# Kernel tuning notes

Measured on AMD Instinct MI355X. Metric: run time of the kernel, lower is better.

## Reference

```python
import jax, jax.numpy as jnp
import numpy as np

N, F_IN, F_OUT = 8192, 256, 128


def setup_inputs() -> dict:
    key = jax.random.key(0)
    k1, k2, k3, k4 = jax.random.split(key, 4)
    h = jax.random.normal(k1, (N, F_IN), dtype=jnp.float32)
    adj = jax.random.randint(k2, (N, N), 0, 2, dtype=jnp.int32)
    # xavier-uniform-like init scales
    w_lim = float(np.sqrt(6.0 / (F_IN + F_OUT)))
    a_lim = float(np.sqrt(6.0 / (2 * F_OUT + 1)))
    W = jax.random.uniform(k3, (F_IN, F_OUT), jnp.float32, -w_lim, w_lim)
    a = jax.random.uniform(k4, (2 * F_OUT, 1), jnp.float32, -a_lim, a_lim)
    return {"h": h, "adj": adj, "W": W, "a": a}


def reference(h, adj, W, a):
    # Wh: [N, F_OUT]
    Wh = h @ W
    # Fused form of the pairwise-concat score: e[i,j] = leakyrelu(Wh_i.a1 + Wh_j.a2)
    a1 = a[:F_OUT]   # [F_OUT, 1]
    a2 = a[F_OUT:]   # [F_OUT, 1]
    s1 = Wh @ a1     # [N, 1]
    s2 = Wh @ a2     # [N, 1]
    e = jax.nn.leaky_relu(s1 + s2.T, negative_slope=0.2)  # [N, N]
    e = jnp.where(adj > 0, e, jnp.float32(-9e15))
    attention = jax.nn.softmax(e, axis=1)
    return attention @ Wh  # [N, F_OUT]
```

## Files before the change

kernel.cpp:

```cpp
#include <hip/hip_runtime.h>

#define N_   8192
#define FIN  256
#define FOUT 128
#define NW   (N_ / 32)

typedef _Float16 f16x8  __attribute__((ext_vector_type(8)));
typedef _Float16 f16x4  __attribute__((ext_vector_type(4)));
typedef float    f32x16 __attribute__((ext_vector_type(16)));
typedef unsigned int uint;

__global__ __launch_bounds__(256) void k_pack(
    const int* __restrict__ adj, uint* __restrict__ bm)
{
    const int wid = (blockIdx.x * 256 + threadIdx.x) >> 6;
    const int l   = threadIdx.x & 63;
    const int4* __restrict__ arow = (const int4*)(adj + (size_t)wid * N_);
    uint* __restrict__ brow = bm + (size_t)wid * NW;

    #pragma unroll 2
    for (int jb = 0; jb < 32; ++jb) {
        int4 av = arow[jb * 64 + l];
        uint nib = (uint)(av.x != 0) | ((uint)(av.y != 0) << 1)
                 | ((uint)(av.z != 0) << 2) | ((uint)(av.w != 0) << 3);
        uint v = nib | (__shfl_xor(nib, 1, 64) << 4);
        v = v | (__shfl_xor(v, 2, 64) << 8);
        v = v | (__shfl_xor(v, 4, 64) << 16);
        if ((l & 7) == 0)
            brow[jb * 8 + (l >> 3)] = v;
    }
}

__global__ __launch_bounds__(256) void k_wh(
    const float* __restrict__ h, const float* __restrict__ W,
    const float* __restrict__ a, float* __restrict__ Wh,
    float* __restrict__ s1, float* __restrict__ s2)
{
    __shared__ float hrow[2][FIN];
    __shared__ float rbuf[2][2][2];
    const int t   = threadIdx.x;
    const int rh  = t >> 7;
    const int c   = t & 127;
    const int row = (blockIdx.x << 1) + rh;

    hrow[rh][c]       = h[(size_t)row * FIN + c];
    hrow[rh][c + 128] = h[(size_t)row * FIN + c + 128];
    __syncthreads();

    float acc = 0.f;
    #pragma unroll 8
    for (int k = 0; k < FIN; ++k)
        acc = fmaf(hrow[rh][k], W[k * FOUT + c], acc);

    Wh[(size_t)row * FOUT + c] = acc;

    float p1 = acc * a[c];
    float p2 = acc * a[FOUT + c];
    #pragma unroll
    for (int off = 32; off; off >>= 1) {
        p1 += __shfl_down(p1, off, 64);
        p2 += __shfl_down(p2, off, 64);
    }
    if ((t & 63) == 0) { rbuf[rh][c >> 6][0] = p1; rbuf[rh][c >> 6][1] = p2; }
    __syncthreads();
    if (c == 0) {
        const float k2 = 1.44269504088896f;
        s1[row] = (rbuf[rh][0][0] + rbuf[rh][1][0]) * k2;
        s2[row] = (rbuf[rh][0][1] + rbuf[rh][1][1]) * k2;
    }
}

__global__ __launch_bounds__(256) void k_tr(
    const float* __restrict__ Wh, _Float16* __restrict__ WhTt)
{
    __shared__ float tile[64][129];
    const int t = threadIdx.x;
    const int rbase = blockIdx.x * 64;

    #pragma unroll
    for (int q = 0; q < 8; ++q) {
        int i4 = q * 256 + t;
        int r  = i4 >> 5;
        int c4 = (i4 & 31) * 4;
        *(float4*)&tile[r][c4] = *(const float4*)&Wh[(size_t)(rbase + r) * FOUT + c4];
    }
    __syncthreads();

    const int c = t >> 1, half = t & 1;
    _Float16 buf[32];
    #pragma unroll
    for (int r = 0; r < 32; ++r) buf[r] = (_Float16)tile[32 * half + r][c];
    _Float16* d0 = WhTt + ((size_t)(rbase >> 4) + 2 * half) * 2048 + c * 16;
    *(f16x8*)(d0)        = *(f16x8*)&buf[0];
    *(f16x8*)(d0 + 8)    = *(f16x8*)&buf[8];
    *(f16x8*)(d0 + 2048)     = *(f16x8*)&buf[16];
    *(f16x8*)(d0 + 2048 + 8) = *(f16x8*)&buf[24];
}

__global__ __launch_bounds__(256, 2) void k_attn(
    const uint* __restrict__ bm, const _Float16* __restrict__ WhTt,
    const float* __restrict__ s1g, const float* __restrict__ s2g,
    _Float16* __restrict__ num_g, float* __restrict__ den_g)
{
    const int t = threadIdx.x;
    const int w = t >> 6, l = t & 63;
    const int n31 = l & 31, h = l >> 5;
    const int shiftH = h << 3;

    const int sp    = blockIdx.x & 7;
    const int rbase = (blockIdx.x >> 3) * 128 + w * 32;
    const int jbase = sp * 1024;

    const int   row = rbase + n31;
    const float s1r = s1g[row];
    const uint*     __restrict__ mrow = bm + (size_t)row * NW + sp * 32;
    const float*    __restrict__ s2p  = s2g + jbase + 8 * h;
    const _Float16* __restrict__ bpt  =
        WhTt + (size_t)(sp * 64) * 2048 + n31 * 16 + 8 * h;

    f32x16 acc0 = {0.f}, acc1 = {0.f}, acc2 = {0.f}, acc3 = {0.f};
    #pragma unroll
    for (int q = 0; q < 16; ++q) { acc0[q]=0.f; acc1[q]=0.f; acc2[q]=0.f; acc3[q]=0.f; }
    float denp = 0.f;

    auto computeP = [&](uint byte, const float4& s0, const float4& s1v) -> f16x8 {
        const float bias = -5.77078016f;
        float m, e;
        f16x8 pv;
        m = s1r + s0.x;  e = fmaxf(m, 0.2f * m); pv[0] = (_Float16)((byte & 1u)   ? __builtin_amdgcn_exp2f(e + bias) : 0.f);
        m = s1r + s0.y;  e = fmaxf(m, 0.2f * m); pv[1] = (_Float16)((byte & 2u)   ? __builtin_amdgcn_exp2f(e + bias) : 0.f);
        m = s1r + s0.z;  e = fmaxf(m, 0.2f * m); pv[2] = (_Float16)((byte & 4u)   ? __builtin_amdgcn_exp2f(e + bias) : 0.f);
        m = s1r + s0.w;  e = fmaxf(m, 0.2f * m); pv[3] = (_Float16)((byte & 8u)   ? __builtin_amdgcn_exp2f(e + bias) : 0.f);
        m = s1r + s1v.x; e = fmaxf(m, 0.2f * m); pv[4] = (_Float16)((byte & 16u)  ? __builtin_amdgcn_exp2f(e + bias) : 0.f);
        m = s1r + s1v.y; e = fmaxf(m, 0.2f * m); pv[5] = (_Float16)((byte & 32u)  ? __builtin_amdgcn_exp2f(e + bias) : 0.f);
        m = s1r + s1v.z; e = fmaxf(m, 0.2f * m); pv[6] = (_Float16)((byte & 64u)  ? __builtin_amdgcn_exp2f(e + bias) : 0.f);
        m = s1r + s1v.w; e = fmaxf(m, 0.2f * m); pv[7] = (_Float16)((byte & 128u) ? __builtin_amdgcn_exp2f(e + bias) : 0.f);
        denp += (float)pv[0] + (float)pv[1] + (float)pv[2] + (float)pv[3]
              + (float)pv[4] + (float)pv[5] + (float)pv[6] + (float)pv[7];
        return pv;
    };

    auto tileStep = [&](int tt, int hi16, uint mk,
                        f16x8& c0, f16x8& c1, f16x8& c2, f16x8& c3,
                        f16x8& d0, f16x8& d1, f16x8& d2, f16x8& d3,
                        float4& sv0, float4& sv1) {
        const int tn = (tt + 1 < 64) ? tt + 1 : 63;
        const _Float16* p = bpt + (size_t)tn * 2048;
        d0 = *(const f16x8*)(p);
        d1 = *(const f16x8*)(p + 512);
        d2 = *(const f16x8*)(p + 1024);
        d3 = *(const f16x8*)(p + 1536);

        f16x8 pv = computeP((mk >> (hi16 + shiftH)) & 255u, sv0, sv1);

        const int ts = (tt + 2 < 64) ? tt + 2 : 63;
        sv0 = *(const float4*)(s2p + ts * 16);
        sv1 = *(const float4*)(s2p + ts * 16 + 4);

        __builtin_amdgcn_s_setprio(1);
        acc0 = __builtin_amdgcn_mfma_f32_32x32x16_f16(pv, c0, acc0, 0, 0, 0);
        acc1 = __builtin_amdgcn_mfma_f32_32x32x16_f16(pv, c1, acc1, 0, 0, 0);
        acc2 = __builtin_amdgcn_mfma_f32_32x32x16_f16(pv, c2, acc2, 0, 0, 0);
        acc3 = __builtin_amdgcn_mfma_f32_32x32x16_f16(pv, c3, acc3, 0, 0, 0);
        __builtin_amdgcn_s_setprio(0);
    };

    uint mk0 = mrow[0], mk1 = mrow[1];
    float4 sA0 = *(const float4*)(s2p);
    float4 sA1 = *(const float4*)(s2p + 4);
    float4 sB0 = *(const float4*)(s2p + 16);
    float4 sB1 = *(const float4*)(s2p + 20);
    f16x8 c0, c1, c2, c3, n0, n1, n2, n3;
    c0 = *(const f16x8*)(bpt);
    c1 = *(const f16x8*)(bpt + 512);
    c2 = *(const f16x8*)(bpt + 1024);
    c3 = *(const f16x8*)(bpt + 1536);

    for (int tt = 0; tt < 64; tt += 4) {
        const int wi = tt >> 1;
        tileStep(tt,     0,  mk0, c0,c1,c2,c3, n0,n1,n2,n3, sA0, sA1);
        tileStep(tt + 1, 16, mk0, n0,n1,n2,n3, c0,c1,c2,c3, sB0, sB1);
        mk0 = mrow[(wi + 2 < 32) ? wi + 2 : 31];
        tileStep(tt + 2, 0,  mk1, c0,c1,c2,c3, n0,n1,n2,n3, sA0, sA1);
        tileStep(tt + 3, 16, mk1, n0,n1,n2,n3, c0,c1,c2,c3, sB0, sB1);
        mk1 = mrow[(wi + 3 < 32) ? wi + 3 : 31];
    }

    denp += __shfl_xor(denp, 32, 64);
    if (l < 32)
        den_g[(size_t)sp * N_ + row] = denp;

    #pragma unroll
    for (int q = 0; q < 16; ++q) {
        const int rl = (q & 3) + 8 * (q >> 2) + 4 * h;
        _Float16* o = num_g + ((size_t)sp * N_ + rbase + rl) * FOUT + n31;
        o[0]  = (_Float16)acc0[q];
        o[32] = (_Float16)acc1[q];
        o[64] = (_Float16)acc2[q];
        o[96] = (_Float16)acc3[q];
    }
}

__global__ __launch_bounds__(256) void k_norm(
    const _Float16* __restrict__ num_g, const float* __restrict__ den_g,
    float* __restrict__ out)
{
    const int idx4 = blockIdx.x * 256 + threadIdx.x;
    const int i  = idx4 >> 5;
    const int c4 = (idx4 & 31) * 4;

    float4 s = {0.f, 0.f, 0.f, 0.f};
    float  d = 0.f;
    #pragma unroll
    for (int sp = 0; sp < 8; ++sp) {
        f16x4 v = *(const f16x4*)(num_g + ((size_t)sp * N_ + i) * FOUT + c4);
        s.x += (float)v[0]; s.y += (float)v[1];
        s.z += (float)v[2]; s.w += (float)v[3];
        d += den_g[(size_t)sp * N_ + i];
    }
    const float inv = 1.f / d;
    float4 o = {s.x * inv, s.y * inv, s.z * inv, s.w * inv};
    *(float4*)&out[(size_t)i * FOUT + c4] = o;
}

extern "C" void kernel_launch(void* const* d_in, const int* in_sizes, int n_in,
                              void* d_out, int out_size, void* d_ws, size_t ws_size,
                              hipStream_t stream) {
    const float* h   = (const float*)d_in[0];
    const int*   adj = (const int*)d_in[1];
    const float* W   = (const float*)d_in[2];
    const float* a   = (const float*)d_in[3];
    float* out = (float*)d_out;

    char* ws = (char*)d_ws;
    float*    Wh   = (float*)ws;
    _Float16* WhTt = (_Float16*)(ws + (4u << 20));
    float*    s1   = (float*)(ws + (6u << 20));
    float*    s2   = (float*)(ws + (6u << 20) + 32768);
    _Float16* num  = (_Float16*)(ws + (7u << 20));
    float*    den  = (float*)(ws + (23u << 20));
    uint*     bmk  = (uint*)(ws + (24u << 20));

    k_pack<<<2048,   256, 0, stream>>>(adj, bmk);
    k_wh  <<<N_ / 2, 256, 0, stream>>>(h, W, a, Wh, s1, s2);
    k_tr  <<<N_ / 64, 256, 0, stream>>>(Wh, WhTt);
    k_attn<<<512,   256, 0, stream>>>(bmk, WhTt, s1, s2, num, den);
    k_norm<<<1024,  256, 0, stream>>>(num, den, out);
}
```

Before: 133.9 us.

## Process two 32-row tiles per wave in attention kernel to reuse Wh fragments

Each wave in k_attn now handles 64 rows instead of 32. It computes two probability fragments per step and runs eight MFMAs against the same loaded Wh B-fragments, which halves global B-operand loads per output row. The grid shrinks from 512 to 256 blocks. The occupancy hint in launch_bounds is dropped, and prefetching moves to a two-tile-ahead X/Y double buffer issued after the MFMAs. In exchange, accumulator register usage doubles and fewer blocks run, which may lower occupancy and CU coverage.

Measured after the change: 136.9 us. 2.2% more time.

```diff
diff --git a/kernel.cpp b/kernel.cpp
--- a/kernel.cpp
+++ b/kernel.cpp
@@ -91,13 +91,13 @@
     #pragma unroll
     for (int r = 0; r < 32; ++r) buf[r] = (_Float16)tile[32 * half + r][c];
     _Float16* d0 = WhTt + ((size_t)(rbase >> 4) + 2 * half) * 2048 + c * 16;
-    *(f16x8*)(d0)        = *(f16x8*)&buf[0];
-    *(f16x8*)(d0 + 8)    = *(f16x8*)&buf[8];
+    *(f16x8*)(d0)            = *(f16x8*)&buf[0];
+    *(f16x8*)(d0 + 8)        = *(f16x8*)&buf[8];
     *(f16x8*)(d0 + 2048)     = *(f16x8*)&buf[16];
     *(f16x8*)(d0 + 2048 + 8) = *(f16x8*)&buf[24];
 }
 
-__global__ __launch_bounds__(256, 2) void k_attn(
+__global__ __launch_bounds__(256) void k_attn(
     const uint* __restrict__ bm, const _Float16* __restrict__ WhTt,
     const float* __restrict__ s1g, const float* __restrict__ s2g,
     _Float16* __restrict__ num_g, float* __restrict__ den_g)
@@ -108,22 +108,28 @@
     const int shiftH = h << 3;
 
     const int sp    = blockIdx.x & 7;
-    const int rbase = (blockIdx.x >> 3) * 128 + w * 32;
+    const int rbase = (blockIdx.x >> 3) * 256 + w * 64;
     const int jbase = sp * 1024;
 
-    const int   row = rbase + n31;
-    const float s1r = s1g[row];
-    const uint*     __restrict__ mrow = bm + (size_t)row * NW + sp * 32;
-    const float*    __restrict__ s2p  = s2g + jbase + 8 * h;
-    const _Float16* __restrict__ bpt  =
+    const int   row0 = rbase + n31, row1 = row0 + 32;
+    const float s1r0 = s1g[row0],  s1r1 = s1g[row1];
+    const uint* __restrict__ mrow0 = bm + (size_t)row0 * NW + sp * 32;
+    const uint* __restrict__ mrow1 = bm + (size_t)row1 * NW + sp * 32;
+    const float*    __restrict__ s2p = s2g + jbase + 8 * h;
+    const _Float16* __restrict__ bpt =
         WhTt + (size_t)(sp * 64) * 2048 + n31 * 16 + 8 * h;
 
     f32x16 acc0 = {0.f}, acc1 = {0.f}, acc2 = {0.f}, acc3 = {0.f};
-    #pragma unroll
-    for (int q = 0; q < 16; ++q) { acc0[q]=0.f; acc1[q]=0.f; acc2[q]=0.f; acc3[q]=0.f; }
-    float denp = 0.f;
-
-    auto computeP = [&](uint byte, const float4& s0, const float4& s1v) -> f16x8 {
+    f32x16 acc4 = {0.f}, acc5 = {0.f}, acc6 = {0.f}, acc7 = {0.f};
+    #pragma unroll
+    for (int q = 0; q < 16; ++q) {
+        acc0[q]=0.f; acc1[q]=0.f; acc2[q]=0.f; acc3[q]=0.f;
+        acc4[q]=0.f; acc5[q]=0.f; acc6[q]=0.f; acc7[q]=0.f;
+    }
+    float denp0 = 0.f, denp1 = 0.f;
+
+    auto computeP = [&](uint byte, const float4& s0, const float4& s1v,
+                        float s1r, float& denp) -> f16x8 {
         const float bias = -5.77078016f;
         float m, e;
         f16x8 pv;
@@ -140,64 +146,81 @@
         return pv;
     };
 
-    auto tileStep = [&](int tt, int hi16, uint mk,
-                        f16x8& c0, f16x8& c1, f16x8& c2, f16x8& c3,
-                        f16x8& d0, f16x8& d1, f16x8& d2, f16x8& d3,
-                        float4& sv0, float4& sv1) {
-        const int tn = (tt + 1 < 64) ? tt + 1 : 63;
-        const _Float16* p = bpt + (size_t)tn * 2048;
-        d0 = *(const f16x8*)(p);
-        d1 = *(const f16x8*)(p + 512);
-        d2 = *(const f16x8*)(p + 1024);
-        d3 = *(const f16x8*)(p + 1536);
-
-        f16x8 pv = computeP((mk >> (hi16 + shiftH)) & 255u, sv0, sv1);
+    auto tileStep = [&](int tt, int hi16, uint mw0, uint mw1,
+                        float4& sv0, float4& sv1,
+                        f16x8& X0, f16x8& X1, f16x8& X2, f16x8& X3) {
+        f16x8 pv0 = computeP((mw0 >> (hi16 + shiftH)) & 255u, sv0, sv1, s1r0, denp0);
+        f16x8 pv1 = computeP((mw1 >> (hi16 + shiftH)) & 255u, sv0, sv1, s1r1, denp1);
 
         const int ts = (tt + 2 < 64) ? tt + 2 : 63;
         sv0 = *(const float4*)(s2p + ts * 16);
         sv1 = *(const float4*)(s2p + ts * 16 + 4);
 
         __builtin_amdgcn_s_setprio(1);
-        acc0 = __builtin_amdgcn_mfma_f32_32x32x16_f16(pv, c0, acc0, 0, 0, 0);
-        acc1 = __builtin_amdgcn_mfma_f32_32x32x16_f16(pv, c1, acc1, 0, 0, 0);
-        acc2 = __builtin_amdgcn_mfma_f32_32x32x16_f16(pv, c2, acc2, 0, 0, 0);
-        acc3 = __builtin_amdgcn_mfma_f32_32x32x16_f16(pv, c3, acc3, 0, 0, 0);
+        acc0 = __builtin_amdgcn_mfma_f32_32x32x16_f16(pv0, X0, acc0, 0, 0, 0);
+        acc1 = __builtin_amdgcn_mfma_f32_32x32x16_f16(pv0, X1, acc1, 0, 0, 0);
+        acc2 = __builtin_amdgcn_mfma_f32_32x32x16_f16(pv0, X2, acc2, 0, 0, 0);
+        acc3 = __builtin_amdgcn_mfma_f32_32x32x16_f16(pv0, X3, acc3, 0, 0, 0);
+        acc4 = __builtin_amdgcn_mfma_f32_32x32x16_f16(pv1, X0, acc4, 0, 0, 0);
+        acc5 = __builtin_amdgcn_mfma_f32_32x32x16_f16(pv1, X1, acc5, 0, 0, 0);
+        acc6 = __builtin_amdgcn_mfma_f32_32x32x16_f16(pv1, X2, acc6, 0, 0, 0);
+        acc7 = __builtin_amdgcn_mfma_f32_32x32x16_f16(pv1, X3, acc7, 0, 0, 0);
         __builtin_amdgcn_s_setprio(0);
+
+        const _Float16* p = bpt + (size_t)ts * 2048;
+        X0 = *(const f16x8*)(p);
+        X1 = *(const f16x8*)(p + 512);
+        X2 = *(const f16x8*)(p + 1024);
+        X3 = *(const f16x8*)(p + 1536);
     };
 
-    uint mk0 = mrow[0], mk1 = mrow[1];
+    uint m00 = mrow0[0], m01 = mrow0[1];
+    uint m10 = mrow1[0], m11 = mrow1[1];
     float4 sA0 = *(const float4*)(s2p);
     float4 sA1 = *(const float4*)(s2p + 4);
     float4 sB0 = *(const float4*)(s2p + 16);
     float4 sB1 = *(const float4*)(s2p + 20);
-    f16x8 c0, c1, c2, c3, n0, n1, n2, n3;
-    c0 = *(const f16x8*)(bpt);
-    c1 = *(const f16x8*)(bpt + 512);
-    c2 = *(const f16x8*)(bpt + 1024);
-    c3 = *(const f16x8*)(bpt + 1536);
+    f16x8 X0 = *(const f16x8*)(bpt);
+    f16x8 X1 = *(const f16x8*)(bpt + 512);
+    f16x8 X2 = *(const f16x8*)(bpt + 1024);
+    f16x8 X3 = *(const f16x8*)(bpt + 1536);
+    f16x8 Y0 = *(const f16x8*)(bpt + 2048);
+    f16x8 Y1 = *(const f16x8*)(bpt + 2048 + 512);
+    f16x8 Y2 = *(const f16x8*)(bpt + 2048 + 1024);
+    f16x8 Y3 = *(const f16x8*)(bpt + 2048 + 1536);
 
     for (int tt = 0; tt < 64; tt += 4) {
         const int wi = tt >> 1;
-        tileStep(tt,     0,  mk0, c0,c1,c2,c3, n0,n1,n2,n3, sA0, sA1);
-        tileStep(tt + 1, 16, mk0, n0,n1,n2,n3, c0,c1,c2,c3, sB0, sB1);
-        mk0 = mrow[(wi + 2 < 32) ? wi + 2 : 31];
-        tileStep(tt + 2, 0,  mk1, c0,c1,c2,c3, n0,n1,n2,n3, sA0, sA1);
-        tileStep(tt + 3, 16, mk1, n0,n1,n2,n3, c0,c1,c2,c3, sB0, sB1);
-        mk1 = mrow[(wi + 3 < 32) ? wi + 3 : 31];
-    }
-
-    denp += __shfl_xor(denp, 32, 64);
-    if (l < 32)
-        den_g[(size_t)sp * N_ + row] = denp;
+        tileStep(tt,     0,  m00, m10, sA0, sA1, X0, X1, X2, X3);
+        tileStep(tt + 1, 16, m00, m10, sB0, sB1, Y0, Y1, Y2, Y3);
+        m00 = mrow0[(wi + 2 < 32) ? wi + 2 : 31];
+        m10 = mrow1[(wi + 2 < 32) ? wi + 2 : 31];
+        tileStep(tt + 2, 0,  m01, m11, sA0, sA1, X0, X1, X2, X3);
+        tileStep(tt + 3, 16, m01, m11, sB0, sB1, Y0, Y1, Y2, Y3);
+        m01 = mrow0[(wi + 3 < 32) ? wi + 3 : 31];
+        m11 = mrow1[(wi + 3 < 32) ? wi + 3 : 31];
+    }
+
+    denp0 += __shfl_xor(denp0, 32, 64);
+    denp1 += __shfl_xor(denp1, 32, 64);
+    if (l < 32) {
+        den_g[(size_t)sp * N_ + row0] = denp0;
+        den_g[(size_t)sp * N_ + row1] = denp1;
+    }
 
     #pragma unroll
     for (int q = 0; q < 16; ++q) {
         const int rl = (q & 3) + 8 * (q >> 2) + 4 * h;
-        _Float16* o = num_g + ((size_t)sp * N_ + rbase + rl) * FOUT + n31;
-        o[0]  = (_Float16)acc0[q];
-        o[32] = (_Float16)acc1[q];
-        o[64] = (_Float16)acc2[q];
-        o[96] = (_Float16)acc3[q];
+        _Float16* o0 = num_g + ((size_t)sp * N_ + rbase + rl) * FOUT + n31;
+        o0[0]  = (_Float16)acc0[q];
+        o0[32] = (_Float16)acc1[q];
+        o0[64] = (_Float16)acc2[q];
+        o0[96] = (_Float16)acc3[q];
+        _Float16* o1 = num_g + ((size_t)sp * N_ + rbase + 32 + rl) * FOUT + n31;
+        o1[0]  = (_Float16)acc4[q];
+        o1[32] = (_Float16)acc5[q];
+        o1[64] = (_Float16)acc6[q];
+        o1[96] = (_Float16)acc7[q];
     }
 }
 
@@ -244,6 +267,6 @@
     k_pack<<<2048,   256, 0, stream>>>(adj, bmk);
     k_wh  <<<N_ / 2, 256, 0, stream>>>(h, W, a, Wh, s1, s2);
     k_tr  <<<N_ / 64, 256, 0, stream>>>(Wh, WhTt);
-    k_attn<<<512,   256, 0, stream>>>(bmk, WhTt, s1, s2, num, den);
+    k_attn<<<256,   256, 0, stream>>>(bmk, WhTt, s1, s2, num, den);
     k_norm<<<1024,  256, 0, stream>>>(num, den, out);
 }
```
